# Performance work log

Hardware: AMD Instinct MI355X
Metric: run time of the kernel (lower is better)

Reference implementation:

```python
import jax, jax.numpy as jnp
import numpy as np
from jax import lax

B, N, C = 1, 4096, 256
NUM_HEADS, TOP_K = 8, 8
HID = 4 * C  # MSFN hidden_dim
EPS = 1e-5


def layer_norm(x, g, b):
    mu = jnp.mean(x, axis=-1, keepdims=True)
    var = jnp.mean((x - mu) ** 2, axis=-1, keepdims=True)
    return (x - mu) / jnp.sqrt(var + EPS) * g + b


def dwconv(x, w, b, pad):
    # x: [B,C,H,W]; w: [O,1,k,k] with feature_group_count=C (torch groups=dim)
    y = lax.conv_general_dilated(x, w, (1, 1), [(pad, pad), (pad, pad)],
                                 feature_group_count=C,
                                 dimension_numbers=("NCHW", "OIHW", "NCHW"))
    return y + b[None, :, None, None]


def setup_inputs() -> dict:
    key = jax.random.key(0)
    ks = jax.random.split(key, 12)
    std = 0.02
    inp = {
        "x": jax.random.normal(ks[0], (B, N, C), jnp.float32),
        "H": 64,
        "W": 64,
        "ln1_g": jnp.ones((C,), jnp.float32),
        "ln1_b": jnp.zeros((C,), jnp.float32),
        "q_w": jax.random.normal(ks[1], (C, C), jnp.float32) * std,
        "q_b": jnp.zeros((C,), jnp.float32),
        "kv_w": jax.random.normal(ks[2], (C, 2 * C), jnp.float32) * std,
        "kv_b": jnp.zeros((2 * C,), jnp.float32),
        "proj_w": jax.random.normal(ks[3], (C, C), jnp.float32) * std,
        "proj_b": jnp.zeros((C,), jnp.float32),
        "ln2_g": jnp.ones((C,), jnp.float32),
        "ln2_b": jnp.zeros((C,), jnp.float32),
        "conv3_w": jax.random.normal(ks[4], (HID, 1, 3, 3), jnp.float32) * np.sqrt(2.0 / (HID * 9 / C)),
        "conv3_b": jnp.zeros((HID,), jnp.float32),
        "conv5_w": jax.random.normal(ks[5], (HID, 1, 5, 5), jnp.float32) * np.sqrt(2.0 / (HID * 25 / C)),
        "conv5_b": jnp.zeros((HID,), jnp.float32),
        "conv1_w": jax.random.normal(ks[6], (C, 2 * HID, 1, 1), jnp.float32) * np.sqrt(2.0 / (C + 2 * HID)),
        "conv1_b": jnp.zeros((C,), jnp.float32),
    }
    return inp


def reference(x, H, W, ln1_g, ln1_b, q_w, q_b, kv_w, kv_b, proj_w, proj_b,
              ln2_g, ln2_b, conv3_w, conv3_b, conv5_w, conv5_b, conv1_w, conv1_b):
    Bh, Nn, Cc = x.shape
    D = Cc // NUM_HEADS
    scale = D ** -0.5

    # --- Dynamic sparse attention ---
    h = layer_norm(x, ln1_g, ln1_b)
    q = jax.nn.relu((h @ q_w + q_b).reshape(Bh, Nn, NUM_HEADS, D).transpose(0, 2, 1, 3))
    kv = (h @ kv_w + kv_b).reshape(Bh, Nn, 2, NUM_HEADS, D).transpose(2, 0, 3, 1, 4)
    k, v = kv[0], kv[1]  # [B,heads,N,D]
    attn = jnp.einsum("bhnd,bhmd->bhnm", q, k) * scale  # full dense map
    _, idx = lax.top_k(attn, TOP_K)  # [B,heads,N,k]
    bi = jnp.arange(Bh)[:, None, None, None]
    hi = jnp.arange(NUM_HEADS)[None, :, None, None]
    ni = jnp.arange(Nn)[None, None, :, None]
    mask = jnp.zeros_like(attn).at[bi, hi, ni, idx].set(1.0)
    # NOTE: matches torch exactly: non-topk entries become 0 (not -inf) pre-softmax
    sa = jax.nn.softmax(attn * mask, axis=-1)
    out = jnp.einsum("bhnm,bhmd->bhnd", sa, v).transpose(0, 2, 1, 3).reshape(Bh, Nn, Cc)
    x = x + (out @ proj_w + proj_b)

    # --- MSFN ---
    h2 = layer_norm(x, ln2_g, ln2_b)
    img = h2.transpose(0, 2, 1).reshape(Bh, Cc, H, W)
    x3 = jax.nn.relu(dwconv(img, conv3_w, conv3_b, 1))
    x5 = jax.nn.relu(dwconv(img, conv5_w, conv5_b, 2))
    cat = jnp.concatenate([x3, x5], axis=1)
    y = lax.conv_general_dilated(cat, conv1_w, (1, 1), [(0, 0), (0, 0)],
                                 dimension_numbers=("NCHW", "OIHW", "NCHW"))
    y = y + conv1_b[None, :, None, None]
    x = x + y.reshape(Bh, Cc, Nn).transpose(0, 2, 1)
    return x
```

## Files before the change

### kernel.cpp

```cpp
#include <hip/hip_runtime.h>
#include <math.h>

#define N_TOK 4096
#define C_DIM 256
#define HEADS 8
#define HDIM  32
#define SCALE 0.17677669529663687f

typedef float f32x4 __attribute__((ext_vector_type(4)));
typedef float f32x2 __attribute__((ext_vector_type(2)));
typedef int   i32x4 __attribute__((ext_vector_type(4)));
typedef __bf16 bf16x8 __attribute__((ext_vector_type(8)));
typedef __bf16 bf16x2 __attribute__((ext_vector_type(2)));

#if defined(__has_builtin)
#if __has_builtin(__builtin_amdgcn_mfma_f32_16x16x32_bf16)
#define HAVE_MFMA_BUILTIN 1
#endif
#if __has_builtin(__builtin_amdgcn_fdot2_f32_bf16)
#define HAVE_DOT2 1
#endif
#endif

__device__ __forceinline__ unsigned short f2bf(float x){
  unsigned u = __float_as_uint(x);
  u += 0x7FFFu + ((u >> 16) & 1u);
  return (unsigned short)(u >> 16);
}

__device__ __forceinline__ size_t pk_idx(int m, int k, int KT){
  return ((size_t)(m >> 4)*KT + (k >> 5))*512 + (((m & 15) + 16*((k >> 3) & 3))*8 + (k & 7));
}

__device__ __forceinline__ unsigned f2key(float s){
  unsigned b = __float_as_uint(s);
  return b ^ ((unsigned)((int)b >> 31) | 0x80000000u);
}
__device__ __forceinline__ unsigned umax_(unsigned a, unsigned b){ return a > b ? a : b; }
__device__ __forceinline__ unsigned umin_(unsigned a, unsigned b){ return a < b ? a : b; }

#define KCMP(A,i,j) { unsigned h_ = umax_(A[i],A[j]); unsigned l_ = umin_(A[i],A[j]); A[i]=h_; A[j]=l_; }

__device__ __forceinline__ void sort8(unsigned (&k)[8]){
  KCMP(k,0,1) KCMP(k,2,3) KCMP(k,4,5) KCMP(k,6,7)
  KCMP(k,0,2) KCMP(k,1,3) KCMP(k,4,6) KCMP(k,5,7)
  KCMP(k,1,2) KCMP(k,5,6)
  KCMP(k,0,4) KCMP(k,1,5) KCMP(k,2,6) KCMP(k,3,7)
  KCMP(k,2,4) KCMP(k,3,5)
  KCMP(k,1,2) KCMP(k,3,4) KCMP(k,5,6)
}

__device__ __forceinline__ void mergetop8(unsigned (&a)[8], const unsigned (&b)[8]){
  #pragma unroll
  for (int j=0;j<8;++j) a[j] = umax_(a[j], b[7-j]);
  KCMP(a,0,4) KCMP(a,1,5) KCMP(a,2,6) KCMP(a,3,7)
  KCMP(a,0,2) KCMP(a,1,3) KCMP(a,4,6) KCMP(a,5,7)
  KCMP(a,0,1) KCMP(a,2,3) KCMP(a,4,5) KCMP(a,6,7)
}

template<int MLO, int MHI>
__device__ __forceinline__ void merge_keys(unsigned (&k)[8]){
  #pragma unroll
  for (int m=MLO; m<=MHI; m<<=1){
    unsigned o[8];
    #pragma unroll
    for (int j=0;j<8;++j) o[j] = (unsigned)__shfl_xor((int)k[j], m);
    #pragma unroll
    for (int j=0;j<8;++j) k[j] = umax_(k[j], o[7-j]);
    KCMP(k,0,4) KCMP(k,1,5) KCMP(k,2,6) KCMP(k,3,7)
    KCMP(k,0,2) KCMP(k,1,3) KCMP(k,4,6) KCMP(k,5,7)
    KCMP(k,0,1) KCMP(k,2,3) KCMP(k,4,5) KCMP(k,6,7)
  }
}

__device__ __forceinline__ f32x4 mfma16(i32x4 a, i32x4 b, f32x4 c){
#ifdef HAVE_MFMA_BUILTIN
  return __builtin_amdgcn_mfma_f32_16x16x32_bf16(
      __builtin_bit_cast(bf16x8, a), __builtin_bit_cast(bf16x8, b), c, 0, 0, 0);
#else
  f32x4 d;
  asm volatile("v_mfma_f32_16x16x32_bf16 %0, %1, %2, %3\n\ts_nop 7\n\ts_nop 3"
               : "=&v"(d) : "v"(a), "v"(b), "v"(c));
  return d;
#endif
}

#ifdef HAVE_DOT2
struct QCtx { unsigned q[16]; };
__device__ __forceinline__ void qload(QCtx& qc, const unsigned short* qrow){
  #pragma unroll
  for (int i=0;i<4;++i){
    i32x4 qv = *(const i32x4*)(qrow + i*8);
    #pragma unroll
    for (int j=0;j<4;++j) qc.q[i*4+j] = (unsigned)qv[j];
  }
}
__device__ __forceinline__ float dot32(const i32x4& k0, const i32x4& k1,
                                       const i32x4& k2, const i32x4& k3, const QCtx& qc){
  float s = 0.f;
  #pragma unroll
  for (int q=0;q<4;++q){
    const i32x4& kv = (q==0)?k0 : (q==1)?k1 : (q==2)?k2 : k3;
    #pragma unroll
    for (int j=0;j<4;++j)
      s = __builtin_amdgcn_fdot2_f32_bf16(__builtin_bit_cast(bf16x2, (unsigned)kv[j]),
                                          __builtin_bit_cast(bf16x2, qc.q[q*4+j]), s, false);
  }
  return s;
}
#else
struct QCtx { f32x2 q[16]; };
__device__ __forceinline__ void qload(QCtx& qc, const unsigned short* qrow){
  #pragma unroll
  for (int i=0;i<4;++i){
    i32x4 qv = *(const i32x4*)(qrow + i*8);
    #pragma unroll
    for (int j=0;j<4;++j){
      unsigned u = (unsigned)qv[j];
      f32x2 p; p.x = __uint_as_float(u << 16); p.y = __uint_as_float(u & 0xFFFF0000u);
      qc.q[i*4+j] = p;
    }
  }
}
__device__ __forceinline__ float dot32(const i32x4& k0, const i32x4& k1,
                                       const i32x4& k2, const i32x4& k3, const QCtx& qc){
  f32x2 acc = {0.f, 0.f};
  #pragma unroll
  for (int q=0;q<4;++q){
    const i32x4& kv = (q==0)?k0 : (q==1)?k1 : (q==2)?k2 : k3;
    #pragma unroll
    for (int j=0;j<4;++j){
      unsigned u = (unsigned)kv[j];
      f32x2 p; p.x = __uint_as_float(u << 16); p.y = __uint_as_float(u & 0xFFFF0000u);
      acc += p * qc.q[q*4+j];
    }
  }
  return acc.x + acc.y;
}
#endif

template<int TO_PACK>
__global__ __launch_bounds__(256) void ln_kernel(const float* __restrict__ x,
    const float* __restrict__ g, const float* __restrict__ b,
    float* __restrict__ outF, unsigned short* __restrict__ outP)
{
  int row = blockIdx.x, c = threadIdx.x;
  float v = x[(size_t)row*C_DIM + c];
  float s1 = v, s2 = v*v;
  #pragma unroll
  for (int off=1; off<64; off<<=1){
    s1 += __shfl_xor(s1, off);
    s2 += __shfl_xor(s2, off);
  }
  __shared__ float r1[4], r2[4];
  int wv = c >> 6;
  if ((c & 63) == 0){ r1[wv] = s1; r2[wv] = s2; }
  __syncthreads();
  s1 = r1[0]+r1[1]+r1[2]+r1[3];
  s2 = r2[0]+r2[1]+r2[2]+r2[3];
  float mu  = s1 * (1.0f/C_DIM);
  float var = s2 * (1.0f/C_DIM) - mu*mu;
  float inv = 1.0f / sqrtf(var + 1e-5f);
  float o = (v - mu) * inv * g[c] + b[c];
  if (TO_PACK) outP[pk_idx(row, c, 8)] = f2bf(o);
  else         outF[(size_t)row*C_DIM + c] = o;
}

__global__ __launch_bounds__(256) void transpose_k(const float* __restrict__ src,
    float* __restrict__ dstF, int R, int Cc)
{
  __shared__ float t[64][65];
  int c0 = blockIdx.x*64, r0 = blockIdx.y*64;
  int x = threadIdx.x & 63, ys = threadIdx.x >> 6;
  #pragma unroll
  for (int i=0;i<16;++i){
    int r = ys + i*4;
    t[r][x] = src[(size_t)(r0+r)*Cc + c0 + x];
  }
  __syncthreads();
  #pragma unroll
  for (int i=0;i<16;++i){
    int rr = ys + i*4;
    dstF[(size_t)(c0+rr)*R + r0 + x] = t[x][rr];
  }
}

__global__ __launch_bounds__(256) void transpose_pack(const float* __restrict__ src,
    unsigned short* __restrict__ dstP, int Cc, int nbase, int KT)
{
  __shared__ float t[64][65];
  int c0 = blockIdx.x*64, r0 = blockIdx.y*64;
  int x = threadIdx.x & 63, ys = threadIdx.x >> 6;
  #pragma unroll
  for (int i=0;i<16;++i){
    int r = ys + i*4;
    t[r][x] = src[(size_t)(r0+r)*Cc + c0 + x];
  }
  __syncthreads();
  #pragma unroll
  for (int i=0;i<16;++i){
    int rr = ys + i*4;
    int n = nbase + c0 + rr;
    int k = r0 + x;
    dstP[pk_idx(n, k, KT)] = f2bf(t[x][rr]);
  }
}

__global__ __launch_bounds__(256) void pack_w1(const float* __restrict__ w1,
                                               unsigned short* __restrict__ w1p)
{
  int blk = blockIdx.x;
  int tid = threadIdx.x;
  int lane = tid >> 2;
  int j = (tid & 3) * 2;
  int n = (blk >> 6)*16 + (lane & 15);
  int k = (blk & 63)*32 + (lane >> 4)*8 + j;
  unsigned lo = f2bf(w1[(size_t)n*2048 + k]);
  unsigned hi = f2bf(w1[(size_t)n*2048 + k + 1]);
  *(unsigned*)(w1p + (size_t)blk*512 + lane*8 + j) = lo | (hi << 16);
}

__global__ __launch_bounds__(256) void repack_k(const unsigned short* __restrict__ kbf,
                                               unsigned short* __restrict__ kpack)
{
  int blk = blockIdx.x;
  int t = blk & 255, h = blk >> 8;
  int tid = threadIdx.x;
  int lane = tid >> 2;
  int j = (tid & 3) * 2;
  int l16 = lane & 15, lg = lane >> 4;
  unsigned val = *(const unsigned*)(kbf + (size_t)(t*16 + l16)*C_DIM + h*HDIM + lg*8 + j);
  *(unsigned*)(kpack + (size_t)blk*512 + tid*2) = val;
}

#define LDT(p, i) (*(const i32x4*)((p) + (size_t)(i)*512))

template<int KTT, int KTC, int NPAIR>
__global__ __launch_bounds__(128, 2) void gemm_packed(
    const unsigned short* __restrict__ Ap, const unsigned short* __restrict__ Bp,
    const float* __restrict__ bias, const float* __restrict__ resid,
    float* __restrict__ outF, float* __restrict__ pbuf)
{
  int wave = threadIdx.x >> 6, lane = threadIdx.x & 63;
  int l16 = lane & 15, lg = lane >> 4;
  int mt = blockIdx.x*2 + wave;
  int nt0 = blockIdx.y * NPAIR;
  int z = blockIdx.z;
  const unsigned short* ap  = Ap + ((size_t)mt*KTT  + z*KTC)*512 + lane*8;
  const unsigned short* bp0 = Bp + ((size_t)nt0*KTT + z*KTC)*512 + lane*8;
  const unsigned short* bp1 = Bp + ((size_t)(nt0+1)*KTT + z*KTC)*512 + lane*8;
  f32x4 acc0 = {0.f,0.f,0.f,0.f}, acc1 = acc0;

  i32x4 A0 = LDT(ap,0), A1 = LDT(ap,1), A2 = LDT(ap,2), A3 = LDT(ap,3);
  i32x4 B0 = LDT(bp0,0), B1 = LDT(bp0,1), B2 = LDT(bp0,2), B3 = LDT(bp0,3);
  i32x4 C0, C1, C2, C3;
  if (NPAIR == 2){ C0 = LDT(bp1,0); C1 = LDT(bp1,1); C2 = LDT(bp1,2); C3 = LDT(bp1,3); }
  #pragma unroll
  for (int kt = 0; kt < KTC; ++kt){
    const int nk = (kt + 4 < KTC) ? (kt + 4) : (KTC - 1);
    switch (kt & 3){
      case 0: acc0 = mfma16(A0, B0, acc0); if (NPAIR==2) acc1 = mfma16(A0, C0, acc1);
              A0 = LDT(ap,nk); B0 = LDT(bp0,nk); if (NPAIR==2) C0 = LDT(bp1,nk); break;
      case 1: acc0 = mfma16(A1, B1, acc0); if (NPAIR==2) acc1 = mfma16(A1, C1, acc1);
              A1 = LDT(ap,nk); B1 = LDT(bp0,nk); if (NPAIR==2) C1 = LDT(bp1,nk); break;
      case 2: acc0 = mfma16(A2, B2, acc0); if (NPAIR==2) acc1 = mfma16(A2, C2, acc1);
              A2 = LDT(ap,nk); B2 = LDT(bp0,nk); if (NPAIR==2) C2 = LDT(bp1,nk); break;
      case 3: acc0 = mfma16(A3, B3, acc0); if (NPAIR==2) acc1 = mfma16(A3, C3, acc1);
              A3 = LDT(ap,nk); B3 = LDT(bp0,nk); if (NPAIR==2) C3 = LDT(bp1,nk); break;
    }
  }
  if (pbuf){
    float* pb = pbuf + (size_t)z * (N_TOK*C_DIM);
    #pragma unroll
    for (int f=0; f<NPAIR; ++f){
      f32x4 acc = f ? acc1 : acc0;
      int n = (nt0 + f)*16 + l16;
      #pragma unroll
      for (int r=0;r<4;++r)
        pb[(size_t)(mt*16 + lg*4 + r)*C_DIM + n] = acc[r];
    }
  } else {
    #pragma unroll
    for (int f=0; f<NPAIR; ++f){
      f32x4 acc = f ? acc1 : acc0;
      int n = (nt0 + f)*16 + l16;
      float bb = bias[n];
      #pragma unroll
      for (int r=0;r<4;++r){
        int m = mt*16 + lg*4 + r;
        float val = acc[r] + bb;
        if (resid) val += resid[(size_t)m*C_DIM + n];
        outF[(size_t)m*C_DIM + n] = val;
      }
    }
  }
}

__global__ __launch_bounds__(128, 2) void gemm_qkv_packed(
    const unsigned short* __restrict__ Ap, const unsigned short* __restrict__ Bp,
    const float* __restrict__ q_b, const float* __restrict__ kv_b,
    unsigned short* __restrict__ qbf, unsigned short* __restrict__ kbf,
    float* __restrict__ vbuf)
{
  int wave = threadIdx.x >> 6, lane = threadIdx.x & 63;
  int l16 = lane & 15, lg = lane >> 4;
  int mt = blockIdx.x*2 + wave;
  int nt = blockIdx.y;
  const unsigned short* ap = Ap + ((size_t)mt*8)*512 + lane*8;
  const unsigned short* bp = Bp + ((size_t)nt*8)*512 + lane*8;
  f32x4 acc = {0.f,0.f,0.f,0.f};
  i32x4 A0 = LDT(ap,0), A1 = LDT(ap,1), A2 = LDT(ap,2), A3 = LDT(ap,3);
  i32x4 B0 = LDT(bp,0), B1 = LDT(bp,1), B2 = LDT(bp,2), B3 = LDT(bp,3);
  #pragma unroll
  for (int kt = 0; kt < 8; ++kt){
    const int nk = (kt + 4 < 8) ? (kt + 4) : 7;
    switch (kt & 3){
      case 0: acc = mfma16(A0, B0, acc); A0 = LDT(ap,nk); B0 = LDT(bp,nk); break;
      case 1: acc = mfma16(A1, B1, acc); A1 = LDT(ap,nk); B1 = LDT(bp,nk); break;
      case 2: acc = mfma16(A2, B2, acc); A2 = LDT(ap,nk); B2 = LDT(bp,nk); break;
      case 3: acc = mfma16(A3, B3, acc); A3 = LDT(ap,nk); B3 = LDT(bp,nk); break;
    }
  }
  int n = nt*16 + l16;
  float bb = (n < 256) ? q_b[n] : kv_b[n-256];
  #pragma unroll
  for (int r=0;r<4;++r){
    int m = mt*16 + lg*4 + r;
    float val = acc[r] + bb;
    if (n < 256)      qbf[(size_t)m*C_DIM + n]        = f2bf(fmaxf(val, 0.f));
    else if (n < 512) kbf[(size_t)m*C_DIM + (n-256)]  = f2bf(val);
    else              vbuf[(size_t)m*C_DIM + (n-512)] = val;
  }
}

__global__ __launch_bounds__(256) void reduce_conv1(const float* __restrict__ pbuf,
    const float* __restrict__ bias, const float* __restrict__ resid,
    float* __restrict__ out)
{
  int i = (blockIdx.x*256 + threadIdx.x) * 4;
  f32x4 a = *(const f32x4*)(pbuf + i);
  f32x4 b = *(const f32x4*)(pbuf + (size_t)N_TOK*C_DIM + i);
  f32x4 r = *(const f32x4*)(resid + i);
  f32x4 bb = *(const f32x4*)(bias + (i & 255));
  *(f32x4*)(out + i) = a + b + r + bb;
}

__global__ __launch_bounds__(256) void colsum_part(const float* __restrict__ v, float* __restrict__ part){
  int b = blockIdx.x, c = threadIdx.x;
  float s = 0.f;
  for (int r=0;r<64;++r) s += v[(size_t)(b*64+r)*C_DIM + c];
  part[b*C_DIM + c] = s;
}
__global__ __launch_bounds__(256) void colsum_final(const float* __restrict__ part, float* __restrict__ sumv){
  int c = threadIdx.x;
  float s = 0.f;
  for (int b=0;b<64;++b) s += part[b*C_DIM + c];
  sumv[c] = s;
}

__global__ __launch_bounds__(256, 4) void attn_kernel(
    const unsigned short* __restrict__ qbf, const unsigned short* __restrict__ kbf,
    const unsigned short* __restrict__ kpack,
    const float* __restrict__ v, const float* __restrict__ sumv,
    unsigned short* __restrict__ outp)
{
  const int head = blockIdx.y;
  const int tid  = threadIdx.x;
  const int wave = tid >> 6, lane = tid & 63;
  const int l16 = lane & 15, lg = lane >> 4;
  const int row0 = blockIdx.x * 32;

  __shared__ unsigned ls[4][2][16][8];
  __shared__ int   gsel[32][8];
  __shared__ float lds_e[32][8];
  __shared__ int   lds_idx[32][8];

  i32x4 qf0 = *(const i32x4*)(qbf + (size_t)(row0      + l16)*C_DIM + head*HDIM + lg*8);
  i32x4 qf1 = *(const i32x4*)(qbf + (size_t)(row0 + 16 + l16)*C_DIM + head*HDIM + lg*8);
  const f32x4 zacc = {0.f,0.f,0.f,0.f};
  const int tbase = wave * 64;
  const unsigned short* kp = kpack + ((size_t)(head*256 + tbase)*64 + lane)*8;

  i32x4 kr0 = *(const i32x4*)(kp);
  i32x4 kr1 = *(const i32x4*)(kp + 512);
  i32x4 kr2 = *(const i32x4*)(kp + 1024);
  i32x4 kr3 = *(const i32x4*)(kp + 1536);
  i32x4 kr4 = *(const i32x4*)(kp + 2048);
  i32x4 kr5 = *(const i32x4*)(kp + 2560);
  i32x4 kr6 = *(const i32x4*)(kp + 3072);
  i32x4 kr7 = *(const i32x4*)(kp + 3584);

  unsigned t0[8], t1[8], g80[8], g81[8];
  #pragma unroll
  for (int j=0;j<8;++j){ t0[j]=0u; t1[j]=0u; }
  const int codebase = 511 - wave*128 - lg;
  #pragma unroll
  for (int g = 0; g < 32; ++g){
    float gm0 = -3e38f, gm1 = -3e38f;
    #pragma unroll
    for (int u = 0; u < 2; ++u){
      const int t = g*2 + u;
      #define USE_SLOT(S) { \
        f32x4 a0 = mfma16(S, qf0, zacc); \
        f32x4 a1 = mfma16(S, qf1, zacc); \
        S = *(const i32x4*)(kp + (size_t)(t+8)*512); \
        gm0 = fmaxf(gm0, fmaxf(fmaxf(a0[0],a0[1]), fmaxf(a0[2],a0[3]))); \
        gm1 = fmaxf(gm1, fmaxf(fmaxf(a1[0],a1[1]), fmaxf(a1[2],a1[3]))); }
      switch (t & 7){
        case 0: USE_SLOT(kr0); break;
        case 1: USE_SLOT(kr1); break;
        case 2: USE_SLOT(kr2); break;
        case 3: USE_SLOT(kr3); break;
        case 4: USE_SLOT(kr4); break;
        case 5: USE_SLOT(kr5); break;
        case 6: USE_SLOT(kr6); break;
        case 7: USE_SLOT(kr7); break;
      }
      #undef USE_SLOT
    }
    unsigned code = (unsigned)(codebase - g*4);
    g80[g & 7] = (f2key(gm0) & 0xFFFFFE00u) | code;
    g81[g & 7] = (f2key(gm1) & 0xFFFFFE00u) | code;
    if ((g & 7) == 7){
      sort8(g80); mergetop8(t0, g80);
      sort8(g81); mergetop8(t1, g81);
    }
  }
  merge_keys<16,32>(t0);
  merge_keys<16,32>(t1);

  if (lg == 0){
    #pragma unroll
    for (int j=0;j<8;++j){ ls[wave][0][l16][j]=t0[j]; ls[wave][1][l16][j]=t1[j]; }
  }
  __syncthreads();

  if (wave < 2){
    unsigned mk[8];
    #pragma unroll
    for (int j=0;j<8;++j) mk[j] = ls[lg][wave][l16][j];
    merge_keys<16,32>(mk);
    if (lg == 0){
      #pragma unroll
      for (int j=0;j<8;++j){
        int gid = 511 - (int)(mk[j] & 511u);
        gsel[wave*16 + l16][j] = (gid >> 2)*32 + (gid & 3)*4;
      }
    }
  }
  __syncthreads();

  const int prow = tid >> 3;
  const int sub  = tid & 7;
  QCtx qc;
  qload(qc, qbf + (size_t)(row0 + prow)*C_DIM + head*HDIM);
  const int base = gsel[prow][sub];
  const unsigned short* kh = kbf + head*HDIM;
  #define COLOF(c) (base + (((c) >> 2) << 4) + ((c) & 3))
  unsigned sv[8];
  #pragma unroll
  for (int j=0;j<8;++j) sv[j] = 0u;
  i32x4 A0,A1,A2,A3, B0,B1,B2,B3;
  { const unsigned short* p = kh + (size_t)COLOF(0)*C_DIM;
    A0 = *(const i32x4*)(p); A1 = *(const i32x4*)(p+8); A2 = *(const i32x4*)(p+16); A3 = *(const i32x4*)(p+24); }
  { const unsigned short* p = kh + (size_t)COLOF(1)*C_DIM;
    B0 = *(const i32x4*)(p); B1 = *(const i32x4*)(p+8); B2 = *(const i32x4*)(p+16); B3 = *(const i32x4*)(p+24); }
  #pragma unroll
  for (int c = 0; c < 8; ++c){
    float s;
    if ((c & 1) == 0){
      s = dot32(A0,A1,A2,A3, qc);
      if (c + 2 < 8){
        const unsigned short* p = kh + (size_t)COLOF(c+2)*C_DIM;
        A0 = *(const i32x4*)(p); A1 = *(const i32x4*)(p+8); A2 = *(const i32x4*)(p+16); A3 = *(const i32x4*)(p+24);
      }
    } else {
      s = dot32(B0,B1,B2,B3, qc);
      if (c + 2 < 8){
        const unsigned short* p = kh + (size_t)COLOF(c+2)*C_DIM;
        B0 = *(const i32x4*)(p); B1 = *(const i32x4*)(p+8); B2 = *(const i32x4*)(p+16); B3 = *(const i32x4*)(p+24);
      }
    }
    int col = COLOF(c);
    unsigned kk = (f2key(s) & 0xFFFFF000u) | (unsigned)(4095 - col);
    #pragma unroll
    for (int j=0;j<8;++j){ unsigned h = umax_(sv[j], kk); kk = umin_(sv[j], kk); sv[j] = h; }
  }
  #undef COLOF
  merge_keys<1,4>(sv);

  {
    int col = 4095 - (int)(sv[sub] & 4095u);
    const unsigned short* krow = kh + (size_t)col*C_DIM;
    i32x4 k0 = *(const i32x4*)(krow);
    i32x4 k1 = *(const i32x4*)(krow+8);
    i32x4 k2 = *(const i32x4*)(krow+16);
    i32x4 k3 = *(const i32x4*)(krow+24);
    float s = dot32(k0,k1,k2,k3, qc);
    lds_e[prow][sub] = expm1f(s*SCALE);
    lds_idx[prow][sub] = col;
  }
  __syncthreads();

  #pragma unroll
  for (int it=0; it<4; ++it){
    int flat = it*256 + tid;
    int rl = flat >> 5, d = flat & 31;
    float num = sumv[head*HDIM + d];
    float den = 4096.0f;
    #pragma unroll
    for (int j=0;j<8;++j){
      float e = lds_e[rl][j];
      den += e;
      num += e * v[(size_t)lds_idx[rl][j]*C_DIM + head*HDIM + d];
    }
    int row = row0 + rl;
    outp[pk_idx(row, head*HDIM + d, 8)] = f2bf(num/den);
  }
}

__global__ __launch_bounds__(256) void dwconv_tiled(const float* __restrict__ img,
    const float* __restrict__ w3, const float* __restrict__ b3,
    const float* __restrict__ w5, const float* __restrict__ b5,
    unsigned short* __restrict__ apack)
{
  __shared__ float tile[8][513];
  int bx = blockIdx.x;
  int ic0 = bx * 8;
  int py0 = blockIdx.y * 4;
  int tid = threadIdx.x;

  #pragma unroll
  for (int i = 0; i < 16; ++i){
    int idx = i*256 + tid;
    int ch  = idx >> 9;
    int rem = idx & 511;
    int ry  = rem >> 6, x = rem & 63;
    int y   = py0 - 2 + ry;
    float v = (y >= 0 && y < 64) ? img[(size_t)(ic0+ch)*4096 + y*64 + x] : 0.f;
    tile[ch][ry*64 + x] = v;
  }
  __syncthreads();

  int o_l  = tid & 31;
  int p_l  = tid >> 5;
  int ic_l = o_l >> 2;
  int o3   = ic0*4 + o_l;
  const float* pl = tile[ic_l];

  float W3[9], W5[25];
  #pragma unroll
  for (int i=0;i<9;++i)  W3[i] = w3[o3*9+i];
  #pragma unroll
  for (int i=0;i<25;++i) W5[i] = w5[o3*25+i];
  float bb3 = b3[o3], bb5 = b5[o3];

  int lane_lo = 16*((o_l >> 3) & 3);
  int elem    = o_l & 7;

  #pragma unroll 4
  for (int it = 0; it < 32; ++it){
    int pp = it*8 + p_l;
    int ly = (pp >> 6) + 2;
    int x  = pp & 63;
    float a3 = bb3, a5 = bb5;
    #pragma unroll
    for (int dy=-2; dy<=2; ++dy){
      #pragma unroll
      for (int dx=-2; dx<=2; ++dx){
        int xx = x + dx;
        float iv = (xx >= 0 && xx < 64) ? pl[(ly+dy)*64 + xx] : 0.f;
        a5 += W5[(dy+2)*5 + dx+2] * iv;
        if (dy>=-1 && dy<=1 && dx>=-1 && dx<=1)
          a3 += W3[(dy+1)*3 + dx+1] * iv;
      }
    }
    int p = (py0 + (pp>>6))*64 + x;
    size_t ad3 = ((size_t)(p >> 4)*64 + bx)*512 + ((p & 15) + lane_lo)*8 + elem;
    apack[ad3]               = f2bf(fmaxf(a3, 0.f));
    apack[ad3 + 32*512]      = f2bf(fmaxf(a5, 0.f));
  }
}

extern "C" void kernel_launch(void* const* d_in, const int* in_sizes, int n_in,
                              void* d_out, int out_size, void* d_ws, size_t ws_size,
                              hipStream_t stream)
{
  (void)in_sizes; (void)n_in; (void)out_size; (void)ws_size;
  const float* x      = (const float*)d_in[0];
  const float* ln1_g  = (const float*)d_in[3];
  const float* ln1_b  = (const float*)d_in[4];
  const float* q_w    = (const float*)d_in[5];
  const float* q_b    = (const float*)d_in[6];
  const float* kv_w   = (const float*)d_in[7];
  const float* kv_b   = (const float*)d_in[8];
  const float* proj_w = (const float*)d_in[9];
  const float* proj_b = (const float*)d_in[10];
  const float* ln2_g  = (const float*)d_in[11];
  const float* ln2_b  = (const float*)d_in[12];
  const float* w3     = (const float*)d_in[13];
  const float* b3     = (const float*)d_in[14];
  const float* w5     = (const float*)d_in[15];
  const float* b5     = (const float*)d_in[16];
  const float* w1     = (const float*)d_in[17];
  const float* b1     = (const float*)d_in[18];
  float* out = (float*)d_out;
  char* ws = (char*)d_ws;

  unsigned short* wAllP = (unsigned short*)(ws + 0x0);
  unsigned short* pwP   = (unsigned short*)(ws + 0x60000);
  unsigned short* w1P   = (unsigned short*)(ws + 0x80000);
  unsigned short* hpack = (unsigned short*)(ws + 0x180000);
  unsigned short* qbf   = (unsigned short*)(ws + 0x380000);
  unsigned short* kbf   = (unsigned short*)(ws + 0x580000);
  float*          vbuf  = (float*)(ws + 0x780000);
  unsigned short* opack = (unsigned short*)(ws + 0xB80000);
  float*          x2    = (float*)(ws + 0xD80000);
  float*          sumv  = (float*)(ws + 0x1180000);
  float*          part  = (float*)(ws + 0x1190000);
  unsigned short* kpack = (unsigned short*)(ws + 0x180000);
  float*          h2    = (float*)(ws + 0x180000);
  float*          h2T   = (float*)(ws + 0x580000);
  float*          pbuf  = (float*)(ws + 0x180000);
  unsigned short* apack = (unsigned short*)(ws + 0x1200000);

  dim3 b256(256), b128(128);

  pack_w1<<<dim3(1024), b256, 0, stream>>>(w1, w1P);
  transpose_pack<<<dim3(4,4), b256, 0, stream>>>(q_w,   wAllP, 256, 0,   8);
  transpose_pack<<<dim3(8,4), b256, 0, stream>>>(kv_w,  wAllP, 512, 256, 8);
  transpose_pack<<<dim3(4,4), b256, 0, stream>>>(proj_w, pwP,  256, 0,   8);

  ln_kernel<1><<<dim3(4096), b256, 0, stream>>>(x, ln1_g, ln1_b, nullptr, hpack);
  gemm_qkv_packed<<<dim3(128,48), b128, 0, stream>>>(hpack, wAllP, q_b, kv_b, qbf, kbf, vbuf);
  repack_k<<<dim3(2048), b256, 0, stream>>>(kbf, kpack);
  colsum_part <<<dim3(64), b256, 0, stream>>>(vbuf, part);
  colsum_final<<<dim3(1),  b256, 0, stream>>>(part, sumv);
  attn_kernel<<<dim3(128,8), b256, 0, stream>>>(qbf, kbf, kpack, vbuf, sumv, opack);
  gemm_packed<8,8,1><<<dim3(128,16,1), b128, 0, stream>>>(opack, pwP, proj_b, x, x2, nullptr);

  ln_kernel<0><<<dim3(4096), b256, 0, stream>>>(x2, ln2_g, ln2_b, h2, nullptr);
  transpose_k<<<dim3(4,64), b256, 0, stream>>>(h2, h2T, 4096, 256);
  dwconv_tiled<<<dim3(32,16), b256, 0, stream>>>(h2T, w3, b3, w5, b5, apack);
  gemm_packed<64,32,2><<<dim3(128,8,2), b128, 0, stream>>>(apack, w1P, nullptr, nullptr, nullptr, pbuf);
  reduce_conv1<<<dim3(1024), b256, 0, stream>>>(pbuf, b1, x2, out);
}
```

Baseline: 138.1 us.

## Fuse K repack into QKV GEMM epilogue and widen GEMM N-tiles

The QKV GEMM epilogue now writes K straight into the packed layout the attention kernel reads, so the separate repack_k launch goes away. hpack moves to a new workspace region because kpack now overlaps it while the GEMM still reads it. The QKV and projection GEMMs each compute two N-tiles per wave, reusing the A fragment and halving the grid. The attention kernel computes each row's softmax denominator reciprocal once in shared memory instead of per output element, at the cost of an extra barrier.

```diff
diff --git a/kernel.cpp b/kernel.cpp
--- a/kernel.cpp
+++ b/kernel.cpp
@@ -218,19 +218,6 @@
   unsigned lo = f2bf(w1[(size_t)n*2048 + k]);
   unsigned hi = f2bf(w1[(size_t)n*2048 + k + 1]);
   *(unsigned*)(w1p + (size_t)blk*512 + lane*8 + j) = lo | (hi << 16);
-}
-
-__global__ __launch_bounds__(256) void repack_k(const unsigned short* __restrict__ kbf,
-                                               unsigned short* __restrict__ kpack)
-{
-  int blk = blockIdx.x;
-  int t = blk & 255, h = blk >> 8;
-  int tid = threadIdx.x;
-  int lane = tid >> 2;
-  int j = (tid & 3) * 2;
-  int l16 = lane & 15, lg = lane >> 4;
-  unsigned val = *(const unsigned*)(kbf + (size_t)(t*16 + l16)*C_DIM + h*HDIM + lg*8 + j);
-  *(unsigned*)(kpack + (size_t)blk*512 + tid*2) = val;
 }
 
 #define LDT(p, i) (*(const i32x4*)((p) + (size_t)(i)*512))
@@ -300,36 +287,53 @@
     const unsigned short* __restrict__ Ap, const unsigned short* __restrict__ Bp,
     const float* __restrict__ q_b, const float* __restrict__ kv_b,
     unsigned short* __restrict__ qbf, unsigned short* __restrict__ kbf,
-    float* __restrict__ vbuf)
+    float* __restrict__ vbuf, unsigned short* __restrict__ kpackW)
 {
   int wave = threadIdx.x >> 6, lane = threadIdx.x & 63;
   int l16 = lane & 15, lg = lane >> 4;
   int mt = blockIdx.x*2 + wave;
-  int nt = blockIdx.y;
-  const unsigned short* ap = Ap + ((size_t)mt*8)*512 + lane*8;
-  const unsigned short* bp = Bp + ((size_t)nt*8)*512 + lane*8;
-  f32x4 acc = {0.f,0.f,0.f,0.f};
+  int nt0 = blockIdx.y * 2;
+  const unsigned short* ap  = Ap + ((size_t)mt*8)*512 + lane*8;
+  const unsigned short* bp0 = Bp + ((size_t)nt0*8)*512 + lane*8;
+  const unsigned short* bp1 = Bp + ((size_t)(nt0+1)*8)*512 + lane*8;
+  f32x4 acc0 = {0.f,0.f,0.f,0.f}, acc1 = acc0;
   i32x4 A0 = LDT(ap,0), A1 = LDT(ap,1), A2 = LDT(ap,2), A3 = LDT(ap,3);
-  i32x4 B0 = LDT(bp,0), B1 = LDT(bp,1), B2 = LDT(bp,2), B3 = LDT(bp,3);
+  i32x4 B0 = LDT(bp0,0), B1 = LDT(bp0,1), B2 = LDT(bp0,2), B3 = LDT(bp0,3);
+  i32x4 C0 = LDT(bp1,0), C1 = LDT(bp1,1), C2 = LDT(bp1,2), C3 = LDT(bp1,3);
   #pragma unroll
   for (int kt = 0; kt < 8; ++kt){
     const int nk = (kt + 4 < 8) ? (kt + 4) : 7;
     switch (kt & 3){
-      case 0: acc = mfma16(A0, B0, acc); A0 = LDT(ap,nk); B0 = LDT(bp,nk); break;
-      case 1: acc = mfma16(A1, B1, acc); A1 = LDT(ap,nk); B1 = LDT(bp,nk); break;
-      case 2: acc = mfma16(A2, B2, acc); A2 = LDT(ap,nk); B2 = LDT(bp,nk); break;
-      case 3: acc = mfma16(A3, B3, acc); A3 = LDT(ap,nk); B3 = LDT(bp,nk); break;
-    }
-  }
-  int n = nt*16 + l16;
-  float bb = (n < 256) ? q_b[n] : kv_b[n-256];
-  #pragma unroll
-  for (int r=0;r<4;++r){
-    int m = mt*16 + lg*4 + r;
-    float val = acc[r] + bb;
-    if (n < 256)      qbf[(size_t)m*C_DIM + n]        = f2bf(fmaxf(val, 0.f));
-    else if (n < 512) kbf[(size_t)m*C_DIM + (n-256)]  = f2bf(val);
-    else              vbuf[(size_t)m*C_DIM + (n-512)] = val;
+      case 0: acc0 = mfma16(A0, B0, acc0); acc1 = mfma16(A0, C0, acc1);
+              A0 = LDT(ap,nk); B0 = LDT(bp0,nk); C0 = LDT(bp1,nk); break;
+      case 1: acc0 = mfma16(A1, B1, acc0); acc1 = mfma16(A1, C1, acc1);
+              A1 = LDT(ap,nk); B1 = LDT(bp0,nk); C1 = LDT(bp1,nk); break;
+      case 2: acc0 = mfma16(A2, B2, acc0); acc1 = mfma16(A2, C2, acc1);
+              A2 = LDT(ap,nk); B2 = LDT(bp0,nk); C2 = LDT(bp1,nk); break;
+      case 3: acc0 = mfma16(A3, B3, acc0); acc1 = mfma16(A3, C3, acc1);
+              A3 = LDT(ap,nk); B3 = LDT(bp0,nk); C3 = LDT(bp1,nk); break;
+    }
+  }
+  #pragma unroll
+  for (int f=0; f<2; ++f){
+    f32x4 acc = f ? acc1 : acc0;
+    int n = (nt0 + f)*16 + l16;
+    float bb = (n < 256) ? q_b[n] : kv_b[n-256];
+    #pragma unroll
+    for (int r=0;r<4;++r){
+      int m = mt*16 + lg*4 + r;
+      float val = acc[r] + bb;
+      if (n < 256){
+        qbf[(size_t)m*C_DIM + n] = f2bf(fmaxf(val, 0.f));
+      } else if (n < 512){
+        int ch = n - 256;
+        unsigned short bv = f2bf(val);
+        kbf[(size_t)m*C_DIM + ch] = bv;
+        kpackW[((size_t)((ch >> 5)*256 + mt)*64 + (lg*4 + r) + 16*((ch >> 3) & 3))*8 + (ch & 7)] = bv;
+      } else {
+        vbuf[(size_t)m*C_DIM + (n-512)] = val;
+      }
+    }
   }
 }
 
@@ -374,6 +378,7 @@
   __shared__ int   gsel[32][8];
   __shared__ float lds_e[32][8];
   __shared__ int   lds_idx[32][8];
+  __shared__ float lds_rd[32];
 
   i32x4 qf0 = *(const i32x4*)(qbf + (size_t)(row0      + l16)*C_DIM + head*HDIM + lg*8);
   i32x4 qf1 = *(const i32x4*)(qbf + (size_t)(row0 + 16 + l16)*C_DIM + head*HDIM + lg*8);
@@ -502,20 +507,24 @@
   }
   __syncthreads();
 
+  if (tid < 32){
+    float den = 4096.0f;
+    #pragma unroll
+    for (int j=0;j<8;++j) den += lds_e[tid][j];
+    lds_rd[tid] = 1.0f / den;
+  }
+  __syncthreads();
+
   #pragma unroll
   for (int it=0; it<4; ++it){
     int flat = it*256 + tid;
     int rl = flat >> 5, d = flat & 31;
     float num = sumv[head*HDIM + d];
-    float den = 4096.0f;
-    #pragma unroll
-    for (int j=0;j<8;++j){
-      float e = lds_e[rl][j];
-      den += e;
-      num += e * v[(size_t)lds_idx[rl][j]*C_DIM + head*HDIM + d];
-    }
+    #pragma unroll
+    for (int j=0;j<8;++j)
+      num += lds_e[rl][j] * v[(size_t)lds_idx[rl][j]*C_DIM + head*HDIM + d];
     int row = row0 + rl;
-    outp[pk_idx(row, head*HDIM + d, 8)] = f2bf(num/den);
+    outp[pk_idx(row, head*HDIM + d, 8)] = f2bf(num * lds_rd[rl]);
   }
 }
 
@@ -577,8 +586,8 @@
     }
     int p = (py0 + (pp>>6))*64 + x;
     size_t ad3 = ((size_t)(p >> 4)*64 + bx)*512 + ((p & 15) + lane_lo)*8 + elem;
-    apack[ad3]               = f2bf(fmaxf(a3, 0.f));
-    apack[ad3 + 32*512]      = f2bf(fmaxf(a5, 0.f));
+    apack[ad3]          = f2bf(fmaxf(a3, 0.f));
+    apack[ad3 + 32*512] = f2bf(fmaxf(a5, 0.f));
   }
 }
 
@@ -610,15 +619,15 @@
   unsigned short* wAllP = (unsigned short*)(ws + 0x0);
   unsigned short* pwP   = (unsigned short*)(ws + 0x60000);
   unsigned short* w1P   = (unsigned short*)(ws + 0x80000);
-  unsigned short* hpack = (unsigned short*)(ws + 0x180000);
+  unsigned short* kpack = (unsigned short*)(ws + 0x180000);
   unsigned short* qbf   = (unsigned short*)(ws + 0x380000);
   unsigned short* kbf   = (unsigned short*)(ws + 0x580000);
   float*          vbuf  = (float*)(ws + 0x780000);
   unsigned short* opack = (unsigned short*)(ws + 0xB80000);
   float*          x2    = (float*)(ws + 0xD80000);
+  unsigned short* hpack = (unsigned short*)(ws + 0xD80000);
   float*          sumv  = (float*)(ws + 0x1180000);
   float*          part  = (float*)(ws + 0x1190000);
-  unsigned short* kpack = (unsigned short*)(ws + 0x180000);
   float*          h2    = (float*)(ws + 0x180000);
   float*          h2T   = (float*)(ws + 0x580000);
   float*          pbuf  = (float*)(ws + 0x180000);
@@ -632,12 +641,11 @@
   transpose_pack<<<dim3(4,4), b256, 0, stream>>>(proj_w, pwP,  256, 0,   8);
 
   ln_kernel<1><<<dim3(4096), b256, 0, stream>>>(x, ln1_g, ln1_b, nullptr, hpack);
-  gemm_qkv_packed<<<dim3(128,48), b128, 0, stream>>>(hpack, wAllP, q_b, kv_b, qbf, kbf, vbuf);
-  repack_k<<<dim3(2048), b256, 0, stream>>>(kbf, kpack);
+  gemm_qkv_packed<<<dim3(128,24), b128, 0, stream>>>(hpack, wAllP, q_b, kv_b, qbf, kbf, vbuf, kpack);
   colsum_part <<<dim3(64), b256, 0, stream>>>(vbuf, part);
   colsum_final<<<dim3(1),  b256, 0, stream>>>(part, sumv);
   attn_kernel<<<dim3(128,8), b256, 0, stream>>>(qbf, kbf, kpack, vbuf, sumv, opack);
-  gemm_packed<8,8,1><<<dim3(128,16,1), b128, 0, stream>>>(opack, pwP, proj_b, x, x2, nullptr);
+  gemm_packed<8,8,2><<<dim3(128,8,1), b128, 0, stream>>>(opack, pwP, proj_b, x, x2, nullptr);
 
   ln_kernel<0><<<dim3(4096), b256, 0, stream>>>(x2, ln2_g, ln2_b, h2, nullptr);
   transpose_k<<<dim3(4,64), b256, 0, stream>>>(h2, h2T, 4096, 256);
```

Measured after the change: 135.6 us. About the same (-1.8%).
